# Kernel optimization log

Hardware: AMD Instinct MI355X
Metric: run time of the kernel (lower is better)

Reference implementation:

```python
import jax, jax.numpy as jnp
import numpy as np

N = 50000      # nodes
E = 800000     # edges (avg degree 16)
D_IN = 256
H = 128
D_OUT = 64
L = 3
EPS = 1e-5


def setup_inputs() -> dict:
    key = jax.random.key(0)
    ks = jax.random.split(key, 12)
    s = 0.05
    x = jax.random.normal(ks[0], (N, D_IN), jnp.float32)
    edge_index = jax.random.randint(ks[1], (2, E), 0, N, dtype=jnp.int32)
    edge_attr = jax.random.normal(ks[2], (E,), jnp.float32)
    # in / out projections
    W_in = jax.random.normal(ks[3], (D_IN, H), jnp.float32) * s
    b_in = jnp.zeros((H,), jnp.float32)
    W_out = jax.random.normal(ks[4], (H, D_OUT), jnp.float32) * s
    # per-layer ResGatedGraphConv params (stacked over L layers)
    Wk = jax.random.normal(ks[5], (L, H, H), jnp.float32) * s
    Wq = jax.random.normal(ks[6], (L, H, H), jnp.float32) * s
    Wv = jax.random.normal(ks[7], (L, H, H), jnp.float32) * s
    Ws = jax.random.normal(ks[8], (L, H, H), jnp.float32) * s  # lin_skip (no bias)
    We = jax.random.normal(ks[9], (L, 1, H), jnp.float32) * s  # lin_edge
    bk = jnp.zeros((L, H), jnp.float32)
    bq = jnp.zeros((L, H), jnp.float32)
    bv = jnp.zeros((L, H), jnp.float32)
    be = jnp.zeros((L, H), jnp.float32)
    b_gcn = jnp.zeros((L, H), jnp.float32)  # conv bias
    gamma = jnp.ones((L, H), jnp.float32)
    beta = jnp.zeros((L, H), jnp.float32)
    return {
        "x": x, "edge_attr": edge_attr,
        "W_in": W_in, "b_in": b_in,
        "Wk": Wk, "bk": bk, "Wq": Wq, "bq": bq, "Wv": Wv, "bv": bv,
        "We": We, "be": be, "Ws": Ws, "b_gcn": b_gcn,
        "gamma": gamma, "beta": beta, "W_out": W_out,
        "edge_index": edge_index,
    }


def _layernorm(h, g, b):
    mu = jnp.mean(h, axis=-1, keepdims=True)
    var = jnp.mean((h - mu) ** 2, axis=-1, keepdims=True)
    return (h - mu) * jax.lax.rsqrt(var + EPS) * g + b


def reference(x, edge_attr, W_in, b_in, Wk, bk, Wq, bq, Wv, bv, We, be, Ws,
              b_gcn, gamma, beta, W_out, edge_index):
    src = edge_index[0]  # x_j (source)
    dst = edge_index[1]  # x_i (target)
    ea = edge_attr[:, None]  # [E, 1]
    h = x @ W_in + b_in  # dropout_prob = 0 -> identity
    for l in range(L):
        k = h @ Wk[l] + bk[l]          # lin_key(x_i basis)  [N, H]
        q = h @ Wq[l] + bq[l]          # lin_query(x_j)      [N, H]
        v = h @ Wv[l] + bv[l]          # lin_value(x_j)      [N, H]
        e = ea @ We[l] + be[l]         # lin_edge            [E, H]
        # PyG message: sigmoid((k_i+e) + (q_j+e)) * (v_j+e)
        gate = jax.nn.sigmoid(k[dst] + q[src] + 2.0 * e)
        msg = gate * (v[src] + e)      # [E, H]
        agg = jax.ops.segment_sum(msg, dst, num_segments=N)  # add-aggregation
        h = agg + h @ Ws[l] + b_gcn[l]  # root weight + bias
        h = _layernorm(h, gamma[l], beta[l])
        h = jax.nn.gelu(h, approximate=False)  # torch nn.GELU default (erf)
    return h @ W_out  # out_proj, bias=False
```

## Files before the change

kernel.cpp:

```cpp
#include <hip/hip_runtime.h>

#define N_NODES 50000
#define NPAD    50048
#define E_EDGES 800000
#define DIN 256
#define H 128
#define DOUT 64
#define EPSF 1e-5f
#define NBLK 196
#define RT   1563

typedef __bf16 bf16x8 __attribute__((ext_vector_type(8)));
typedef float  f32x4  __attribute__((ext_vector_type(4)));
typedef float  f32x2  __attribute__((ext_vector_type(2)));
typedef unsigned short ushort_t;
typedef unsigned int   uint_t;

#define L2E 1.4426950408889634f
#define LN2 0.6931471805599453f

#if __has_builtin(__builtin_amdgcn_exp2f)
#define EXP2F(x) __builtin_amdgcn_exp2f(x)
#else
#define EXP2F(x) __expf((x) * LN2)
#endif

__device__ inline float bf2f(uint_t u) {
    union { uint_t i; float f; } v; v.i = u << 16; return v.f;
}
__device__ inline ushort_t f2bf(float f) {
    uint_t u = __float_as_uint(f);
    uint_t r = (u + 0x7fffu + ((u >> 16) & 1u)) >> 16;
    return (ushort_t)r;
}

#if __has_builtin(__builtin_amdgcn_cvt_f32_fp8)
#define FP8DEC(u, s) __builtin_amdgcn_cvt_f32_fp8((uint_t)(u), (s))
#else
__device__ inline float fp8_dec_sw(uint_t b) {
    uint_t s = (b & 0x80u) << 24;
    uint_t em = b & 0x7fu;
    if (em < 8u) return __uint_as_float(s);
    uint_t ex = (em >> 3) + 120u;
    uint_t mn = (em & 7u) << 20;
    return __uint_as_float(s | (ex << 23) | mn);
}
#define FP8DEC(u, s) fp8_dec_sw(((uint_t)(u) >> (8 * (s))) & 0xffu)
#endif

#if __has_builtin(__builtin_amdgcn_cvt_pk_f32_fp8)
__device__ __forceinline__ f32x2 cvtpk_q(uint_t u) {
    auto r = __builtin_amdgcn_cvt_pk_f32_fp8(u, false);
    f32x2 o; o.x = r[0]; o.y = r[1]; return o;
}
#else
__device__ __forceinline__ f32x2 cvtpk_q(uint_t u) {
    f32x2 r; r.x = FP8DEC(u, 0); r.y = FP8DEC(u, 1); return r;
}
#endif

#if __has_builtin(__builtin_amdgcn_cvt_pk_fp8_f32)
__device__ inline uint_t fp8_pk(float a, float b) {
    return (uint_t)__builtin_amdgcn_cvt_pk_fp8_f32(a, b, 0, false) & 0xffffu;
}
#else
__device__ inline uint_t fp8_enc_sw(float f) {
    uint_t u = __float_as_uint(f);
    uint_t s = (u >> 24) & 0x80u;
    uint_t a = u & 0x7fffffffu;
    if (a < 0x3c800000u) return s;
    if (a > 0x43e00000u) a = 0x43e00000u;
    uint_t r = a + 0x7ffffu + ((a >> 20) & 1u);
    uint_t ex = (r >> 23) - 120u;
    uint_t mn = (r >> 20) & 7u;
    return s | (ex << 3) | mn;
}
__device__ inline uint_t fp8_pk(float a, float b) {
    return fp8_enc_sw(a) | (fp8_enc_sw(b) << 8);
}
#endif

__global__ __launch_bounds__(256) void k_convx(const float* __restrict__ x, ushort_t* __restrict__ xb)
{
    int i = blockIdx.x * 256 + threadIdx.x;
    float4 v = ((const float4*)x)[i];
    ushort4 o;
    o.x = f2bf(v.x); o.y = f2bf(v.y); o.z = f2bf(v.z); o.w = f2bf(v.w);
    ((ushort4*)xb)[i] = o;
}

__global__ __launch_bounds__(256) void k_pack(const float* __restrict__ Wk, const float* __restrict__ Wq,
                                              const float* __restrict__ Wv, const float* __restrict__ Ws,
                                              const float* __restrict__ W_in, const float* __restrict__ W_out,
                                              ushort_t* __restrict__ Bq, ushort_t* __restrict__ Bin,
                                              ushort_t* __restrict__ Bout)
{
    int t = blockIdx.x * 256 + threadIdx.x;
    if (t < 196608) {
        int l = t >> 16;
        int r = t & 65535;
        int c = r >> 7;
        int k = r & 127;
        int m = c >> 7;
        int cm = c & 127;
        const float* W = (m == 0) ? Wk : (m == 1) ? Wq : (m == 2) ? Wv : Ws;
        Bq[t] = f2bf(W[(size_t)l * H * H + k * H + cm]);
    } else if (t < 229376) {
        int t2 = t - 196608;
        int c = t2 >> 8;
        int k = t2 & 255;
        Bin[t2] = f2bf(W_in[k * H + c]);
    } else {
        int t3 = t - 229376;
        int c = t3 >> 7;
        int k = t3 & 127;
        Bout[t3] = f2bf(W_out[k * DOUT + c]);
    }
}

__global__ __launch_bounds__(256) void k_in_mfma(const ushort_t* __restrict__ xb,
                                                 const ushort_t* __restrict__ Bin,
                                                 const float* __restrict__ b_in,
                                                 ushort_t* __restrict__ hb)
{
    int gw = blockIdx.x * 4 + (threadIdx.x >> 6);
    int lane = threadIdx.x & 63;
    int rt = gw >> 2, c32 = (gw & 3) * 32;
    int r0 = rt * 32;
    const ushort_t* Ap = xb + (size_t)(r0 + (lane & 15)) * DIN + 8 * (lane >> 4);
    const ushort_t* Bp = Bin + (size_t)(c32 + (lane & 15)) * DIN + 8 * (lane >> 4);
    f32x4 acc[2][2];
    #pragma unroll
    for (int rb = 0; rb < 2; ++rb)
        #pragma unroll
        for (int nf = 0; nf < 2; ++nf) acc[rb][nf] = (f32x4){0.f, 0.f, 0.f, 0.f};
    #pragma unroll
    for (int ks = 0; ks < 8; ++ks) {
        bf16x8 a0 = *(const bf16x8*)(Ap + ks * 32);
        bf16x8 a1 = *(const bf16x8*)(Ap + 16 * DIN + ks * 32);
        bf16x8 b0 = *(const bf16x8*)(Bp + ks * 32);
        bf16x8 b1 = *(const bf16x8*)(Bp + 16 * DIN + ks * 32);
        acc[0][0] = __builtin_amdgcn_mfma_f32_16x16x32_bf16(a0, b0, acc[0][0], 0, 0, 0);
        acc[1][0] = __builtin_amdgcn_mfma_f32_16x16x32_bf16(a1, b0, acc[1][0], 0, 0, 0);
        acc[0][1] = __builtin_amdgcn_mfma_f32_16x16x32_bf16(a0, b1, acc[0][1], 0, 0, 0);
        acc[1][1] = __builtin_amdgcn_mfma_f32_16x16x32_bf16(a1, b1, acc[1][1], 0, 0, 0);
    }
    int rowoff = (lane >> 4) << 2;
    #pragma unroll
    for (int nf = 0; nf < 2; ++nf) {
        int col = c32 + nf * 16 + (lane & 15);
        float bb = b_in[col];
        #pragma unroll
        for (int rb = 0; rb < 2; ++rb)
            #pragma unroll
            for (int j = 0; j < 4; ++j)
                hb[(size_t)(r0 + rb * 16 + rowoff + j) * H + col] = f2bf(acc[rb][nf][j] + bb);
    }
}

__global__ __launch_bounds__(256) void k_qkvs_mfma(const ushort_t* __restrict__ hb,
                                                   const ushort_t* __restrict__ Bq,
                                                   const float* __restrict__ bk, const float* __restrict__ bq,
                                                   const float* __restrict__ bv, const float* __restrict__ bs,
                                                   ushort_t* __restrict__ qf8, uint_t* __restrict__ vb,
                                                   uint_t* __restrict__ ks)
{
    int gw = blockIdx.x * 4 + (threadIdx.x >> 6);
    int lane = threadIdx.x & 63;
    int rt = gw >> 3, cfg = gw & 7;
    int pair = cfg >> 2, c32 = (cfg & 3) * 32;
    int r0 = rt * 32;
    const ushort_t* Ap = hb + (size_t)(r0 + (lane & 15)) * H + 8 * (lane >> 4);
    int cb0 = pair ? 0   : 128;
    int cb1 = pair ? 384 : 256;
    const ushort_t* Bp0 = Bq + (size_t)(cb0 + c32 + (lane & 15)) * H + 8 * (lane >> 4);
    const ushort_t* Bp1 = Bq + (size_t)(cb1 + c32 + (lane & 15)) * H + 8 * (lane >> 4);
    f32x4 acc[2][2][2];
    #pragma unroll
    for (int rb = 0; rb < 2; ++rb)
        #pragma unroll
        for (int m = 0; m < 2; ++m)
            #pragma unroll
            for (int nf = 0; nf < 2; ++nf) acc[rb][m][nf] = (f32x4){0.f, 0.f, 0.f, 0.f};
    #pragma unroll
    for (int kk = 0; kk < 4; ++kk) {
        bf16x8 a0 = *(const bf16x8*)(Ap + kk * 32);
        bf16x8 a1 = *(const bf16x8*)(Ap + 16 * H + kk * 32);
        #pragma unroll
        for (int nf = 0; nf < 2; ++nf) {
            bf16x8 b0 = *(const bf16x8*)(Bp0 + nf * 16 * H + kk * 32);
            bf16x8 b1 = *(const bf16x8*)(Bp1 + nf * 16 * H + kk * 32);
            acc[0][0][nf] = __builtin_amdgcn_mfma_f32_16x16x32_bf16(a0, b0, acc[0][0][nf], 0, 0, 0);
            acc[1][0][nf] = __builtin_amdgcn_mfma_f32_16x16x32_bf16(a1, b0, acc[1][0][nf], 0, 0, 0);
            acc[0][1][nf] = __builtin_amdgcn_mfma_f32_16x16x32_bf16(a0, b1, acc[0][1][nf], 0, 0, 0);
            acc[1][1][nf] = __builtin_amdgcn_mfma_f32_16x16x32_bf16(a1, b1, acc[1][1][nf], 0, 0, 0);
        }
    }
    int rowoff = (lane >> 4) << 2;
    int l15 = lane & 15;
    if (pair == 0) {
        int col_lo = c32 + l15, col_hi = col_lo + 16;
        int e = (c32 >> 1) + l15;
        float bql = bq[col_lo], bqh = bq[col_hi];
        float bvl = bv[col_lo], bvh = bv[col_hi];
        #pragma unroll
        for (int rb = 0; rb < 2; ++rb)
            #pragma unroll
            for (int j = 0; j < 4; ++j) {
                size_t row = r0 + rb * 16 + rowoff + j;
                float ql = (acc[rb][0][0][j] + bql) * L2E;
                float qh = (acc[rb][0][1][j] + bqh) * L2E;
                qf8[row * 64 + e] = (ushort_t)fp8_pk(ql, qh);
                uint_t vl = f2bf(acc[rb][1][0][j] + bvl);
                uint_t vh = f2bf(acc[rb][1][1][j] + bvh);
                vb[row * 64 + e] = (vh << 16) | vl;
            }
    } else {
        #pragma unroll
        for (int nf = 0; nf < 2; ++nf) {
            int col = c32 + nf * 16 + l15;
            float bbk = bk[col], bbs = bs[col];
            #pragma unroll
            for (int rb = 0; rb < 2; ++rb)
                #pragma unroll
                for (int j = 0; j < 4; ++j) {
                    size_t row = r0 + rb * 16 + rowoff + j;
                    uint_t kkv = f2bf((acc[rb][0][nf][j] + bbk) * L2E);
                    uint_t ssv = f2bf(acc[rb][1][nf][j] + bbs);
                    ks[row * H + col] = (ssv << 16) | kkv;
                }
        }
    }
}

__global__ __launch_bounds__(256) void k_hist(const int* __restrict__ ei, int* __restrict__ deg)
{
    int e = blockIdx.x * 256 + threadIdx.x;
    int dst = ei[E_EDGES + e];
    atomicAdd(&deg[dst], 1);
}

__global__ __launch_bounds__(256) void k_bsum(const int* __restrict__ deg, int* __restrict__ bsum)
{
    __shared__ int ws[4];
    int t = threadIdx.x;
    int i = blockIdx.x * 256 + t;
    int v = (i < N_NODES) ? deg[i] : 0;
    #pragma unroll
    for (int off = 32; off > 0; off >>= 1) v += __shfl_down(v, off);
    if ((t & 63) == 0) ws[t >> 6] = v;
    __syncthreads();
    if (t == 0) bsum[blockIdx.x] = ws[0] + ws[1] + ws[2] + ws[3];
}

__global__ __launch_bounds__(256) void k_bscan(const int* __restrict__ bsum, int* __restrict__ boff)
{
    __shared__ int ws[4];
    int t = threadIdx.x;
    int v = (t < NBLK) ? bsum[t] : 0;
    int lane = t & 63, wid = t >> 6;
    int inc = v;
    #pragma unroll
    for (int off = 1; off < 64; off <<= 1) {
        int u = __shfl_up(inc, off);
        if (lane >= off) inc += u;
    }
    if (lane == 63) ws[wid] = inc;
    __syncthreads();
    if (t == 0) {
        int s = 0;
        #pragma unroll
        for (int w = 0; w < 4; ++w) { int x = ws[w]; ws[w] = s; s += x; }
    }
    __syncthreads();
    if (t < NBLK) boff[t] = inc - v + ws[wid];
}

__global__ __launch_bounds__(256) void k_rowptr(const int* __restrict__ deg,
                                                const int* __restrict__ boff,
                                                int* __restrict__ rowptr)
{
    __shared__ int ws[4];
    int t = threadIdx.x;
    int i = blockIdx.x * 256 + t;
    int v = (i < N_NODES) ? deg[i] : 0;
    int lane = t & 63, wid = t >> 6;
    int inc = v;
    #pragma unroll
    for (int off = 1; off < 64; off <<= 1) {
        int u = __shfl_up(inc, off);
        if (lane >= off) inc += u;
    }
    if (lane == 63) ws[wid] = inc;
    __syncthreads();
    if (t == 0) {
        int s = 0;
        #pragma unroll
        for (int w = 0; w < 4; ++w) { int x = ws[w]; ws[w] = s; s += x; }
    }
    __syncthreads();
    int excl = inc - v + ws[wid] + boff[blockIdx.x];
    if (i < N_NODES) rowptr[i] = excl;
    if (i == N_NODES - 1) rowptr[N_NODES] = excl + v;
}

__global__ __launch_bounds__(256) void k_scatter(const int* __restrict__ ei,
                                                 const float* __restrict__ ea,
                                                 const int* __restrict__ rowptr,
                                                 int* __restrict__ fill,
                                                 uint2* __restrict__ csr)
{
    int e = blockIdx.x * 256 + threadIdx.x;
    int src = ei[e];
    int dst = ei[E_EDGES + e];
    int pos = rowptr[dst] + atomicAdd(&fill[dst], 1);
    csr[pos] = make_uint2((uint_t)src, __float_as_uint(ea[e]));
}

__device__ __forceinline__ void edge_acc(uint_t qw, uint_t uv, float ea,
                                         f32x2 we2, f32x2 be2, f32x2 kd2, f32x2& acc)
{
    f32x2 q = cvtpk_q(qw);
    f32x2 v;
    v.x = __uint_as_float(uv << 16);
    v.y = __uint_as_float(uv & 0xffff0000u);
    f32x2 av; av.x = ea; av.y = ea;
    f32x2 ep = __builtin_elementwise_fma(av, we2, be2);
    f32x2 g  = __builtin_elementwise_fma((f32x2){2.f, 2.f}, ep, kd2 + q);
    f32x2 ex; ex.x = EXP2F(-g.x); ex.y = EXP2F(-g.y);
    f32x2 d = ex + (f32x2){1.f, 1.f};
    f32x2 sg; sg.x = __builtin_amdgcn_rcpf(d.x); sg.y = __builtin_amdgcn_rcpf(d.y);
    f32x2 m = __builtin_elementwise_fma((f32x2){LN2, LN2}, ep, v);
    acc = __builtin_elementwise_fma(sg, m, acc);
}

__global__ __launch_bounds__(256) void k_agg_ln(const int* __restrict__ rowptr,
                                                const uint2* __restrict__ csr,
                                                const ushort_t* __restrict__ qf8,
                                                const uint_t* __restrict__ vb,
                                                const uint_t* __restrict__ ks,
                                                const float* __restrict__ We,
                                                const float* __restrict__ be,
                                                const float* __restrict__ gamma,
                                                const float* __restrict__ beta,
                                                ushort_t* __restrict__ hout)
{
    int tid = threadIdx.x;
    int lane = tid & 63;
    int node = __builtin_amdgcn_readfirstlane(blockIdx.x * 4 + (tid >> 6));
    int flo = ((lane >> 4) << 5) + (lane & 15);
    int fhi = flo + 16;

    f32x2 we2, be2, kd2, acc;
    we2.x = We[flo] * L2E; we2.y = We[fhi] * L2E;
    be2.x = be[flo] * L2E; be2.y = be[fhi] * L2E;
    uint_t klo = ks[(size_t)node * H + flo];
    uint_t khi = ks[(size_t)node * H + fhi];
    kd2.x = bf2f(klo & 0xffffu); kd2.y = bf2f(khi & 0xffffu);
    acc.x = bf2f(klo >> 16);     acc.y = bf2f(khi >> 16);
    int p = rowptr[node];
    int pend = rowptr[node + 1];

#define GATH(QW, UV, A, C) { \
    A = __uint_as_float((C).y); \
    const ushort_t* qrow_ = qf8 + ((size_t)(C).x << 6); \
    const uint_t*   vrow_ = vb  + ((size_t)(C).x << 6); \
    QW = qrow_[lane]; \
    UV = vrow_[lane]; }

    while (p + 8 <= pend) {
        uint2 c0 = csr[p],     c1 = csr[p + 1], c2 = csr[p + 2], c3 = csr[p + 3];
        uint2 c4 = csr[p + 4], c5 = csr[p + 5], c6 = csr[p + 6], c7 = csr[p + 7];
        uint_t w0, w1, w2, w3, w4, w5, w6, w7;
        uint_t u0, u1, u2, u3, u4, u5, u6, u7;
        float a0, a1, a2, a3, a4, a5, a6, a7;
        GATH(w0, u0, a0, c0); GATH(w1, u1, a1, c1); GATH(w2, u2, a2, c2); GATH(w3, u3, a3, c3);
        GATH(w4, u4, a4, c4); GATH(w5, u5, a5, c5); GATH(w6, u6, a6, c6); GATH(w7, u7, a7, c7);
        edge_acc(w0, u0, a0, we2, be2, kd2, acc);
        edge_acc(w1, u1, a1, we2, be2, kd2, acc);
        edge_acc(w2, u2, a2, we2, be2, kd2, acc);
        edge_acc(w3, u3, a3, we2, be2, kd2, acc);
        edge_acc(w4, u4, a4, we2, be2, kd2, acc);
        edge_acc(w5, u5, a5, we2, be2, kd2, acc);
        edge_acc(w6, u6, a6, we2, be2, kd2, acc);
        edge_acc(w7, u7, a7, we2, be2, kd2, acc);
        p += 8;
    }
    if (p + 4 <= pend) {
        uint2 c0 = csr[p], c1 = csr[p + 1], c2 = csr[p + 2], c3 = csr[p + 3];
        uint_t w0, w1, w2, w3;
        uint_t u0, u1, u2, u3;
        float a0, a1, a2, a3;
        GATH(w0, u0, a0, c0); GATH(w1, u1, a1, c1); GATH(w2, u2, a2, c2); GATH(w3, u3, a3, c3);
        edge_acc(w0, u0, a0, we2, be2, kd2, acc);
        edge_acc(w1, u1, a1, we2, be2, kd2, acc);
        edge_acc(w2, u2, a2, we2, be2, kd2, acc);
        edge_acc(w3, u3, a3, we2, be2, kd2, acc);
        p += 4;
    }
    for (; p < pend; ++p) {
        uint2 c = csr[p];
        uint_t qw, uv; float a;
        GATH(qw, uv, a, c);
        edge_acc(qw, uv, a, we2, be2, kd2, acc);
    }
#undef GATH

    float s  = acc.x + acc.y;
    float s2 = acc.x * acc.x + acc.y * acc.y;
    #pragma unroll
    for (int off = 32; off > 0; off >>= 1) {
        s  += __shfl_down(s, off);
        s2 += __shfl_down(s2, off);
    }
    s  = __shfl(s, 0);
    s2 = __shfl(s2, 0);
    float mu  = s * (1.f / H);
    float var = s2 * (1.f / H) - mu * mu;
    float rstd = rsqrtf(var + EPSF);
    float glo = gamma[flo], ghi = gamma[fhi];
    float blo = beta[flo],  bhi = beta[fhi];
    float y0 = (acc.x - mu) * rstd * glo + blo;
    float y1 = (acc.y - mu) * rstd * ghi + bhi;
    y0 = 0.5f * y0 * (1.f + erff(y0 * 0.70710678118f));
    y1 = 0.5f * y1 * (1.f + erff(y1 * 0.70710678118f));
    hout[(size_t)node * H + flo] = f2bf(y0);
    hout[(size_t)node * H + fhi] = f2bf(y1);
}

__global__ __launch_bounds__(256) void k_out_mfma(const ushort_t* __restrict__ hb,
                                                  const ushort_t* __restrict__ Bout,
                                                  float* __restrict__ out)
{
    int gw = blockIdx.x * 4 + (threadIdx.x >> 6);
    if (gw >= 6250) return;
    int lane = threadIdx.x & 63;
    int rg = gw >> 1, cg = gw & 1;
    int r0 = rg * 16, c0 = cg * 32;
    const ushort_t* Ap = hb + (size_t)(r0 + (lane & 15)) * H + 8 * (lane >> 4);
    const ushort_t* Bp = Bout + (size_t)(c0 + (lane & 15)) * H + 8 * (lane >> 4);
    f32x4 acc[2];
    acc[0] = (f32x4){0.f, 0.f, 0.f, 0.f};
    acc[1] = (f32x4){0.f, 0.f, 0.f, 0.f};
    #pragma unroll
    for (int kk = 0; kk < 4; ++kk) {
        bf16x8 a = *(const bf16x8*)(Ap + kk * 32);
        bf16x8 b0 = *(const bf16x8*)(Bp + kk * 32);
        bf16x8 b1 = *(const bf16x8*)(Bp + 16 * H + kk * 32);
        acc[0] = __builtin_amdgcn_mfma_f32_16x16x32_bf16(a, b0, acc[0], 0, 0, 0);
        acc[1] = __builtin_amdgcn_mfma_f32_16x16x32_bf16(a, b1, acc[1], 0, 0, 0);
    }
    int rowb = r0 + ((lane >> 4) << 2);
    #pragma unroll
    for (int nf = 0; nf < 2; ++nf) {
        int col = c0 + nf * 16 + (lane & 15);
        #pragma unroll
        for (int j = 0; j < 4; ++j)
            out[(size_t)(rowb + j) * DOUT + col] = acc[nf][j];
    }
}

extern "C" void kernel_launch(void* const* d_in, const int* in_sizes, int n_in,
                              void* d_out, int out_size, void* d_ws, size_t ws_size,
                              hipStream_t stream) {
    const float* x         = (const float*)d_in[0];
    const float* edge_attr = (const float*)d_in[1];
    const float* W_in      = (const float*)d_in[2];
    const float* b_in      = (const float*)d_in[3];
    const float* Wk        = (const float*)d_in[4];
    const float* bk        = (const float*)d_in[5];
    const float* Wq        = (const float*)d_in[6];
    const float* bq        = (const float*)d_in[7];
    const float* Wv        = (const float*)d_in[8];
    const float* bv        = (const float*)d_in[9];
    const float* We        = (const float*)d_in[10];
    const float* be        = (const float*)d_in[11];
    const float* Ws        = (const float*)d_in[12];
    const float* b_gcn     = (const float*)d_in[13];
    const float* gamma     = (const float*)d_in[14];
    const float* beta      = (const float*)d_in[15];
    const float* W_out     = (const float*)d_in[16];
    const int*   edge_index= (const int*)d_in[17];
    float* out = (float*)d_out;

    char* wsb = (char*)d_ws;
    ushort_t* hb  = (ushort_t*)wsb;                  wsb += (size_t)NPAD * H * 2;
    ushort_t* qf8 = (ushort_t*)wsb;                  wsb += (size_t)NPAD * 64 * 2;
    uint_t*   vb  = (uint_t*)wsb;                    wsb += (size_t)NPAD * 64 * 4;
    uint_t*   ks  = (uint_t*)wsb;                    wsb += (size_t)NPAD * H * 4;
    ushort_t* xb  = (ushort_t*)wsb;                  wsb += (size_t)NPAD * DIN * 2;
    ushort_t* Bq  = (ushort_t*)wsb;                  wsb += 3 * 512 * 128 * 2;
    ushort_t* Bin = (ushort_t*)wsb;                  wsb += 128 * 256 * 2;
    ushort_t* Bout= (ushort_t*)wsb;                  wsb += 64 * 128 * 2;
    uint2* csr    = (uint2*)wsb;                     wsb += (size_t)E_EDGES * 8;
    int*   deg    = (int*)wsb;                       wsb += N_NODES * 4;
    int*   fill   = (int*)wsb;                       wsb += N_NODES * 4;
    int*   rowptr = (int*)wsb;                       wsb += (N_NODES + 1) * 4;
    int*   bsum   = (int*)wsb;                       wsb += NBLK * 4;
    int*   boff   = (int*)wsb;                       wsb += NBLK * 4;

    (void)hipMemsetAsync(deg, 0, 2 * N_NODES * sizeof(int), stream);
    k_hist<<<E_EDGES / 256, 256, 0, stream>>>(edge_index, deg);
    k_bsum<<<NBLK, 256, 0, stream>>>(deg, bsum);
    k_bscan<<<1, 256, 0, stream>>>(bsum, boff);
    k_rowptr<<<NBLK, 256, 0, stream>>>(deg, boff, rowptr);
    k_scatter<<<E_EDGES / 256, 256, 0, stream>>>(edge_index, edge_attr, rowptr, fill, csr);

    k_convx<<<(N_NODES * DIN / 4 + 255) / 256, 256, 0, stream>>>(x, xb);
    k_pack<<<928, 256, 0, stream>>>(Wk, Wq, Wv, Ws, W_in, W_out, Bq, Bin, Bout);

    k_in_mfma<<<RT, 256, 0, stream>>>(xb, Bin, b_in, hb);
    for (int l = 0; l < 3; ++l) {
        k_qkvs_mfma<<<2 * RT, 256, 0, stream>>>(hb, Bq + (size_t)l * 512 * 128,
                                                bk + l * H, bq + l * H, bv + l * H, b_gcn + l * H,
                                                qf8, vb, ks);
        k_agg_ln<<<N_NODES / 4, 256, 0, stream>>>(rowptr, csr, qf8, vb, ks,
                                                  We + l * H, be + l * H,
                                                  gamma + l * H, beta + l * H, hb);
    }
    k_out_mfma<<<RT, 256, 0, stream>>>(hb, Bout, out);
}
```

Baseline: 417.8 us.

## Merge independent preprocessing kernels into combined block-partitioned launches

The x conversion, weight packing and degree histogram now run as one block-partitioned launch. The input projection GEMM and the CSR scatter run together in a second combined launch. This removes several kernel launches and their serialization gaps, and lets independent work overlap on the device. The scatter path now handles four edges per thread to batch its atomics. The cost is larger, divergent kernels whose register usage is set by the heaviest branch.

```diff
diff --git a/kernel.cpp b/kernel.cpp
--- a/kernel.cpp
+++ b/kernel.cpp
@@ -9,6 +9,10 @@
 #define EPSF 1e-5f
 #define NBLK 196
 #define RT   1563
+#define CVB  12500
+#define PKB  928
+#define HSB  3125
+#define SCB  782
 
 typedef __bf16 bf16x8 __attribute__((ext_vector_type(8)));
 typedef float  f32x4  __attribute__((ext_vector_type(4)));
@@ -80,81 +84,119 @@
 }
 #endif
 
-__global__ __launch_bounds__(256) void k_convx(const float* __restrict__ x, ushort_t* __restrict__ xb)
-{
-    int i = blockIdx.x * 256 + threadIdx.x;
-    float4 v = ((const float4*)x)[i];
-    ushort4 o;
-    o.x = f2bf(v.x); o.y = f2bf(v.y); o.z = f2bf(v.z); o.w = f2bf(v.w);
-    ((ushort4*)xb)[i] = o;
-}
-
-__global__ __launch_bounds__(256) void k_pack(const float* __restrict__ Wk, const float* __restrict__ Wq,
-                                              const float* __restrict__ Wv, const float* __restrict__ Ws,
-                                              const float* __restrict__ W_in, const float* __restrict__ W_out,
-                                              ushort_t* __restrict__ Bq, ushort_t* __restrict__ Bin,
-                                              ushort_t* __restrict__ Bout)
-{
-    int t = blockIdx.x * 256 + threadIdx.x;
-    if (t < 196608) {
-        int l = t >> 16;
-        int r = t & 65535;
-        int c = r >> 7;
-        int k = r & 127;
-        int m = c >> 7;
-        int cm = c & 127;
-        const float* W = (m == 0) ? Wk : (m == 1) ? Wq : (m == 2) ? Wv : Ws;
-        Bq[t] = f2bf(W[(size_t)l * H * H + k * H + cm]);
-    } else if (t < 229376) {
-        int t2 = t - 196608;
-        int c = t2 >> 8;
-        int k = t2 & 255;
-        Bin[t2] = f2bf(W_in[k * H + c]);
+__global__ __launch_bounds__(256) void k_pre(const float* __restrict__ x, ushort_t* __restrict__ xb,
+                                             const float* __restrict__ Wk, const float* __restrict__ Wq,
+                                             const float* __restrict__ Wv, const float* __restrict__ Ws,
+                                             const float* __restrict__ W_in, const float* __restrict__ W_out,
+                                             ushort_t* __restrict__ Bq, ushort_t* __restrict__ Bin,
+                                             ushort_t* __restrict__ Bout,
+                                             const int* __restrict__ ei, int* __restrict__ deg)
+{
+    int b = blockIdx.x;
+    int tid = threadIdx.x;
+    if (b < CVB) {
+        int i = b * 256 + tid;
+        float4 v = ((const float4*)x)[i];
+        ushort4 o;
+        o.x = f2bf(v.x); o.y = f2bf(v.y); o.z = f2bf(v.z); o.w = f2bf(v.w);
+        ((ushort4*)xb)[i] = o;
+    } else if (b < CVB + PKB) {
+        int t = (b - CVB) * 256 + tid;
+        if (t < 196608) {
+            int l = t >> 16;
+            int r = t & 65535;
+            int c = r >> 7;
+            int k = r & 127;
+            int m = c >> 7;
+            int cm = c & 127;
+            const float* W = (m == 0) ? Wk : (m == 1) ? Wq : (m == 2) ? Wv : Ws;
+            Bq[t] = f2bf(W[(size_t)l * H * H + k * H + cm]);
+        } else if (t < 229376) {
+            int t2 = t - 196608;
+            int c = t2 >> 8;
+            int k = t2 & 255;
+            Bin[t2] = f2bf(W_in[k * H + c]);
+        } else {
+            int t3 = t - 229376;
+            int c = t3 >> 7;
+            int k = t3 & 127;
+            Bout[t3] = f2bf(W_out[k * DOUT + c]);
+        }
     } else {
-        int t3 = t - 229376;
-        int c = t3 >> 7;
-        int k = t3 & 127;
-        Bout[t3] = f2bf(W_out[k * DOUT + c]);
-    }
-}
-
-__global__ __launch_bounds__(256) void k_in_mfma(const ushort_t* __restrict__ xb,
-                                                 const ushort_t* __restrict__ Bin,
-                                                 const float* __restrict__ b_in,
-                                                 ushort_t* __restrict__ hb)
-{
-    int gw = blockIdx.x * 4 + (threadIdx.x >> 6);
-    int lane = threadIdx.x & 63;
-    int rt = gw >> 2, c32 = (gw & 3) * 32;
-    int r0 = rt * 32;
-    const ushort_t* Ap = xb + (size_t)(r0 + (lane & 15)) * DIN + 8 * (lane >> 4);
-    const ushort_t* Bp = Bin + (size_t)(c32 + (lane & 15)) * DIN + 8 * (lane >> 4);
-    f32x4 acc[2][2];
-    #pragma unroll
-    for (int rb = 0; rb < 2; ++rb)
-        #pragma unroll
-        for (int nf = 0; nf < 2; ++nf) acc[rb][nf] = (f32x4){0.f, 0.f, 0.f, 0.f};
-    #pragma unroll
-    for (int ks = 0; ks < 8; ++ks) {
-        bf16x8 a0 = *(const bf16x8*)(Ap + ks * 32);
-        bf16x8 a1 = *(const bf16x8*)(Ap + 16 * DIN + ks * 32);
-        bf16x8 b0 = *(const bf16x8*)(Bp + ks * 32);
-        bf16x8 b1 = *(const bf16x8*)(Bp + 16 * DIN + ks * 32);
-        acc[0][0] = __builtin_amdgcn_mfma_f32_16x16x32_bf16(a0, b0, acc[0][0], 0, 0, 0);
-        acc[1][0] = __builtin_amdgcn_mfma_f32_16x16x32_bf16(a1, b0, acc[1][0], 0, 0, 0);
-        acc[0][1] = __builtin_amdgcn_mfma_f32_16x16x32_bf16(a0, b1, acc[0][1], 0, 0, 0);
-        acc[1][1] = __builtin_amdgcn_mfma_f32_16x16x32_bf16(a1, b1, acc[1][1], 0, 0, 0);
-    }
-    int rowoff = (lane >> 4) << 2;
-    #pragma unroll
-    for (int nf = 0; nf < 2; ++nf) {
-        int col = c32 + nf * 16 + (lane & 15);
-        float bb = b_in[col];
+        int e = (b - CVB - PKB) * 256 + tid;
+        int dst = ei[E_EDGES + e];
+        atomicAdd(&deg[dst], 1);
+    }
+}
+
+__global__ __launch_bounds__(256) void k_mid(const ushort_t* __restrict__ xb,
+                                             const ushort_t* __restrict__ Bin,
+                                             const float* __restrict__ b_in,
+                                             ushort_t* __restrict__ hb,
+                                             const int* __restrict__ ei,
+                                             const float* __restrict__ ea,
+                                             const int* __restrict__ rowptr,
+                                             int* __restrict__ fill,
+                                             uint2* __restrict__ csr)
+{
+    int blk = blockIdx.x;
+    int tid = threadIdx.x;
+    if (blk < RT) {
+        int gw = blk * 4 + (tid >> 6);
+        int lane = tid & 63;
+        int rt = gw >> 2, c32 = (gw & 3) * 32;
+        int r0 = rt * 32;
+        const ushort_t* Ap = xb + (size_t)(r0 + (lane & 15)) * DIN + 8 * (lane >> 4);
+        const ushort_t* Bp = Bin + (size_t)(c32 + (lane & 15)) * DIN + 8 * (lane >> 4);
+        f32x4 acc[2][2];
         #pragma unroll
         for (int rb = 0; rb < 2; ++rb)
             #pragma unroll
-            for (int j = 0; j < 4; ++j)
-                hb[(size_t)(r0 + rb * 16 + rowoff + j) * H + col] = f2bf(acc[rb][nf][j] + bb);
+            for (int nf = 0; nf < 2; ++nf) acc[rb][nf] = (f32x4){0.f, 0.f, 0.f, 0.f};
+        #pragma unroll
+        for (int ks = 0; ks < 8; ++ks) {
+            bf16x8 a0 = *(const bf16x8*)(Ap + ks * 32);
+            bf16x8 a1 = *(const bf16x8*)(Ap + 16 * DIN + ks * 32);
+            bf16x8 b0 = *(const bf16x8*)(Bp + ks * 32);
+            bf16x8 b1 = *(const bf16x8*)(Bp + 16 * DIN + ks * 32);
+            acc[0][0] = __builtin_amdgcn_mfma_f32_16x16x32_bf16(a0, b0, acc[0][0], 0, 0, 0);
+            acc[1][0] = __builtin_amdgcn_mfma_f32_16x16x32_bf16(a1, b0, acc[1][0], 0, 0, 0);
+            acc[0][1] = __builtin_amdgcn_mfma_f32_16x16x32_bf16(a0, b1, acc[0][1], 0, 0, 0);
+            acc[1][1] = __builtin_amdgcn_mfma_f32_16x16x32_bf16(a1, b1, acc[1][1], 0, 0, 0);
+        }
+        int rowoff = (lane >> 4) << 2;
+        #pragma unroll
+        for (int nf = 0; nf < 2; ++nf) {
+            int col = c32 + nf * 16 + (lane & 15);
+            float bb = b_in[col];
+            #pragma unroll
+            for (int rb = 0; rb < 2; ++rb)
+                #pragma unroll
+                for (int j = 0; j < 4; ++j)
+                    hb[(size_t)(r0 + rb * 16 + rowoff + j) * H + col] = f2bf(acc[rb][nf][j] + bb);
+        }
+    } else {
+        int e0 = (blk - RT) * 1024 + tid;
+        int src[4], dst[4];
+        float a[4];
+        #pragma unroll
+        for (int k = 0; k < 4; ++k) {
+            int e = e0 + k * 256;
+            if (e < E_EDGES) {
+                src[k] = ei[e];
+                dst[k] = ei[E_EDGES + e];
+                a[k] = ea[e];
+            } else {
+                dst[k] = -1;
+            }
+        }
+        int pos[4];
+        #pragma unroll
+        for (int k = 0; k < 4; ++k)
+            if (dst[k] >= 0) pos[k] = rowptr[dst[k]] + atomicAdd(&fill[dst[k]], 1);
+        #pragma unroll
+        for (int k = 0; k < 4; ++k)
+            if (dst[k] >= 0) csr[pos[k]] = make_uint2((uint_t)src[k], __float_as_uint(a[k]));
     }
 }
 
@@ -233,13 +275,6 @@
     }
 }
 
-__global__ __launch_bounds__(256) void k_hist(const int* __restrict__ ei, int* __restrict__ deg)
-{
-    int e = blockIdx.x * 256 + threadIdx.x;
-    int dst = ei[E_EDGES + e];
-    atomicAdd(&deg[dst], 1);
-}
-
 __global__ __launch_bounds__(256) void k_bsum(const int* __restrict__ deg, int* __restrict__ bsum)
 {
     __shared__ int ws[4];
@@ -302,19 +337,6 @@
     int excl = inc - v + ws[wid] + boff[blockIdx.x];
     if (i < N_NODES) rowptr[i] = excl;
     if (i == N_NODES - 1) rowptr[N_NODES] = excl + v;
-}
-
-__global__ __launch_bounds__(256) void k_scatter(const int* __restrict__ ei,
-                                                 const float* __restrict__ ea,
-                                                 const int* __restrict__ rowptr,
-                                                 int* __restrict__ fill,
-                                                 uint2* __restrict__ csr)
-{
-    int e = blockIdx.x * 256 + threadIdx.x;
-    int src = ei[e];
-    int dst = ei[E_EDGES + e];
-    int pos = rowptr[dst] + atomicAdd(&fill[dst], 1);
-    csr[pos] = make_uint2((uint_t)src, __float_as_uint(ea[e]));
 }
 
 __device__ __forceinline__ void edge_acc(uint_t qw, uint_t uv, float ea,
@@ -500,16 +522,16 @@
     int*   boff   = (int*)wsb;                       wsb += NBLK * 4;
 
     (void)hipMemsetAsync(deg, 0, 2 * N_NODES * sizeof(int), stream);
-    k_hist<<<E_EDGES / 256, 256, 0, stream>>>(edge_index, deg);
+
+    k_pre<<<CVB + PKB + HSB, 256, 0, stream>>>(x, xb, Wk, Wq, Wv, Ws, W_in, W_out,
+                                               Bq, Bin, Bout, edge_index, deg);
     k_bsum<<<NBLK, 256, 0, stream>>>(deg, bsum);
     k_bscan<<<1, 256, 0, stream>>>(bsum, boff);
     k_rowptr<<<NBLK, 256, 0, stream>>>(deg, boff, rowptr);
-    k_scatter<<<E_EDGES / 256, 256, 0, stream>>>(edge_index, edge_attr, rowptr, fill, csr);
-
-    k_convx<<<(N_NODES * DIN / 4 + 255) / 256, 256, 0, stream>>>(x, xb);
-    k_pack<<<928, 256, 0, stream>>>(Wk, Wq, Wv, Ws, W_in, W_out, Bq, Bin, Bout);
-
-    k_in_mfma<<<RT, 256, 0, stream>>>(xb, Bin, b_in, hb);
+
+    k_mid<<<RT + SCB, 256, 0, stream>>>(xb, Bin, b_in, hb,
+                                        edge_index, edge_attr, rowptr, fill, csr);
+
     for (int l = 0; l < 3; ++l) {
         k_qkvs_mfma<<<2 * RT, 256, 0, stream>>>(hb, Bq + (size_t)l * 512 * 128,
                                                 bk + l * H, bq + l * H, bv + l * H, b_gcn + l * H,
```

After: 400.9 us. -4.1%, faster.
